# Kernel optimization log

Measured on AMD Instinct MI355X. Metric: run time of the kernel, lower is better.

Reference implementation:

```python
import jax, jax.numpy as jnp
import numpy as np

B, N, M = 64, 1024, 1024
WIDTH = 1.0
DECAY = 1.0


def setup_inputs() -> dict:
    key = jax.random.key(0)
    k1, k2, k3, k4, k5, k6 = jax.random.split(key, 6)
    # persistence-diagram style points: death = birth + positive lifetime
    bx = jax.random.uniform(k1, (B, N))
    lx = jax.random.uniform(k2, (B, N))
    X = jnp.stack([bx, bx + lx], axis=-1)  # [B, N, 2] (birth, death)
    by = jax.random.uniform(k3, (B, M))
    ly = jax.random.uniform(k4, (B, M))
    Y = jnp.stack([by, by + ly], axis=-1)  # [B, M, 2]
    weights = jax.random.uniform(k5, (B,), minval=0.1, maxval=1.0)
    num_samples = jnp.full((B,), float(N), dtype=jnp.float32)
    return {"X": X, "Y": Y, "weights": weights, "num_samples": num_samples}


def _to_lt(D):
    # (birth, death) -> (birth, lifetime)
    return jnp.stack([D[..., 0], D[..., 1] - D[..., 0]], axis=-1)


def _weighted_kernel_sum(A, Bp, wa, wb):
    # A: [B,n,2], Bp: [B,m,2]; squared euclidean distance, RBF, decay weighting, sum
    d2 = (jnp.sum(A * A, -1)[:, :, None]
          + jnp.sum(Bp * Bp, -1)[:, None, :]
          - 2.0 * jnp.einsum('bnd,bmd->bnm', A, Bp))
    K = jnp.exp(-jnp.maximum(d2, 0.0) / WIDTH)
    return jnp.einsum('bnm,bn,bm->b', K, wa, wb)


def reference(X, Y, weights, num_samples):
    PX = _to_lt(X)  # [B,N,2]
    PY = _to_lt(Y)  # [B,M,2]
    wX = PX[..., 1] ** DECAY  # lifetime^decay; 0 for zero-padded points
    wY = PY[..., 1] ** DECAY
    mmd = (_weighted_kernel_sum(PX, PX, wX, wX)
           - 2.0 * _weighted_kernel_sum(PX, PY, wX, wY)
           + _weighted_kernel_sum(PY, PY, wY, wY))  # [B]
    return jnp.sum(mmd * weights / (num_samples ** 2))
```

## Files before the change

### kernel.cpp

```cpp
#include <hip/hip_runtime.h>


#define LOG2E_F  1.44269504088896340736f
#define SQRT2C_F 1.69864360213614f

struct __align__(16) P4 { float sx, sy, h, w; };

#define NSLOT 64
#define TPB   256

#define ACC_BYTES (NSLOT * 8)
#define PTS_OFF   (ACC_BYTES + 16)

__global__ void prep_kernel(const float* __restrict__ X, const float* __restrict__ Y,
                            P4* __restrict__ PX, P4* __restrict__ PY,
                            int nx_total, int ny_total, double* __restrict__ acc) {
    int i = blockIdx.x * blockDim.x + threadIdx.x;
    if (i < NSLOT) acc[i] = 0.0;
    if (i < nx_total) {
        float2 bd = ((const float2*)X)[i];
        float x = bd.x, l = bd.y - bd.x;
        P4 p; p.sx = SQRT2C_F * x; p.sy = SQRT2C_F * l;
        p.h = -LOG2E_F * fmaf(x, x, l * l); p.w = l;
        PX[i] = p;
    }
    if (i < ny_total) {
        float2 bd = ((const float2*)Y)[i];
        float x = bd.x, l = bd.y - bd.x;
        P4 p; p.sx = SQRT2C_F * x; p.sy = SQRT2C_F * l;
        p.h = -LOG2E_F * fmaf(x, x, l * l); p.w = l;
        PY[i] = p;
    }
}

struct Rows { float asx[4], asy[4], ah[4], aw[4]; };

template<int RS>
__device__ __forceinline__ void strip_full(const P4* __restrict__ tile,
                                           const Rows& A, float* __restrict__ s) {
    #pragma unroll 4
    for (int m = 0; m < 64; ++m) {
        P4 p = tile[m];
        #pragma unroll
        for (int r = RS; r < 4; ++r) {
            float t = fmaf(A.asx[r], p.sx, fmaf(A.asy[r], p.sy, A.ah[r] + p.h));
            s[r] = fmaf(__builtin_amdgcn_exp2f(t), p.w, s[r]);
        }
    }
}

template<int RD>
__device__ __forceinline__ void strip_diag(const P4* __restrict__ tile, int kcap,
                                           const Rows& A, float* __restrict__ s) {
    #pragma unroll 4
    for (int m = 0; m < 64; ++m) {
        P4 p = tile[m];
        float wsel = (m < kcap) ? p.w : 0.0f;
        float t = fmaf(A.asx[RD], p.sx, fmaf(A.asy[RD], p.sy, A.ah[RD] + p.h));
        s[RD] = fmaf(__builtin_amdgcn_exp2f(t), wsel, s[RD]);
    }
}

__device__ __forceinline__ void do_strip_sym(const P4* __restrict__ tile, int j, int w,
                                             int kcap, const Rows& A, float* __restrict__ s) {
    int d = j + 1 - w;
    int rstart = (d <= 0) ? 0 : ((d + 3) >> 2);
    switch (rstart) {
        case 0: strip_full<0>(tile, A, s); break;
        case 1: strip_full<1>(tile, A, s); break;
        case 2: strip_full<2>(tile, A, s); break;
        case 3: strip_full<3>(tile, A, s); break;
        default: break;
    }
    int jd = j - w;
    if (jd >= 0 && jd < 16 && (jd & 3) == 0) {
        switch (jd >> 2) {
            case 0: strip_diag<0>(tile, kcap, A, s); break;
            case 1: strip_diag<1>(tile, kcap, A, s); break;
            case 2: strip_diag<2>(tile, kcap, A, s); break;
            case 3: strip_diag<3>(tile, kcap, A, s); break;
        }
    }
}

__global__ __launch_bounds__(TPB) void mmd_main(
    const P4* __restrict__ PXall, const P4* __restrict__ PYall,
    const float* __restrict__ weights, const float* __restrict__ ns,
    double* __restrict__ acc) {

    const int b    = blockIdx.y;
    const int part = blockIdx.x;
    const int tid  = threadIdx.x;
    const int w    = tid >> 6;
    const int lane = tid & 63;

    __shared__ P4 tiles[4][64];
    __shared__ double redbuf[4];
    P4* tile = tiles[w];

    const P4* __restrict__ PX = PXall + (size_t)b * 1024;
    const P4* __restrict__ PY = PYall + (size_t)b * 1024;

    float thread_val = 0.0f;

    if (part < 16) {
        const int p = part & 7;
        const P4* __restrict__ A = (part < 8) ? PX : PY;
        const int j0 = p, j1 = 15 - p;

        Rows R; float s[4];
        #pragma unroll
        for (int r = 0; r < 4; ++r) {
            P4 a = A[r * 256 + tid];
            R.asx[r] = a.sx; R.asy[r] = a.sy; R.ah[r] = a.h; R.aw[r] = a.w;
            s[r] = 0.0f;
        }

        P4 c0 = A[j0 * 64 + lane];
        P4 c1 = A[j1 * 64 + lane];
        tile[lane] = c0;
        do_strip_sym(tile, j0, w, lane, R, s);
        tile[lane] = c1;
        do_strip_sym(tile, j1, w, lane, R, s);

        float tv = 0.0f;
        #pragma unroll
        for (int r = 0; r < 4; ++r) tv = fmaf(R.aw[r], s[r], tv);
        tv *= 2.0f;
        if (p == 0) {
            #pragma unroll
            for (int r = 0; r < 4; ++r) tv = fmaf(R.aw[r], R.aw[r], tv);
        }
        thread_val = tv;
    } else {
        const int sp = part - 16;
        Rows R; float s[4];
        #pragma unroll
        for (int r = 0; r < 4; ++r) {
            P4 a = PX[r * 256 + tid];
            R.asx[r] = a.sx; R.asy[r] = a.sy; R.ah[r] = a.h; R.aw[r] = a.w;
            s[r] = 0.0f;
        }
        tile[lane] = PY[sp * 64 + lane];
        strip_full<0>(tile, R, s);

        float tv = 0.0f;
        #pragma unroll
        for (int r = 0; r < 4; ++r) tv = fmaf(R.aw[r], s[r], tv);
        thread_val = -2.0f * tv;
    }

    double v = (double)thread_val;
    #pragma unroll
    for (int off = 32; off > 0; off >>= 1) v += __shfl_down(v, off, 64);
    if (lane == 0) redbuf[w] = v;
    __syncthreads();
    if (tid == 0) {
        double tot = (redbuf[0] + redbuf[1]) + (redbuf[2] + redbuf[3]);
        double nsb = (double)ns[b];
        atomicAdd(&acc[b], tot * ((double)weights[b] / (nsb * nsb)));
    }
}

__global__ __launch_bounds__(TPB) void mmd_generic(
    const P4* __restrict__ PXall, const P4* __restrict__ PYall,
    const float* __restrict__ weights, const float* __restrict__ ns,
    int N, int M, double* __restrict__ acc) {

    const int b    = blockIdx.z;
    const int term = blockIdx.y;
    const int seg  = blockIdx.x;

    const P4* __restrict__ A  = (term == 2) ? (PYall + (size_t)b * M) : (PXall + (size_t)b * N);
    const P4* __restrict__ Bp = (term == 0) ? (PXall + (size_t)b * N) : (PYall + (size_t)b * M);
    const int nrows = (term == 2) ? M : N;
    const int mlen  = (term == 0) ? N : M;
    const float sign = (term == 1) ? -2.0f : 1.0f;

    const int mstart = seg * 32;
    const int cnt = (mstart + 32 <= mlen) ? 32 : (mlen > mstart ? mlen - mstart : 0);

    __shared__ P4 tile[32];
    __shared__ double redbuf[TPB / 64];
    if (threadIdx.x < cnt) tile[threadIdx.x] = Bp[mstart + threadIdx.x];
    __syncthreads();

    float thread_val = 0.0f;
    for (int n = threadIdx.x; n < nrows; n += TPB) {
        P4 a = A[n];
        float ss = 0.0f;
        for (int m = 0; m < cnt; ++m) {
            P4 p = tile[m];
            float t = fmaf(a.sx, p.sx, fmaf(a.sy, p.sy, a.h + p.h));
            ss = fmaf(__builtin_amdgcn_exp2f(t), p.w, ss);
        }
        thread_val = fmaf(a.w, ss, thread_val);
    }

    double v = (double)thread_val;
    #pragma unroll
    for (int off = 32; off > 0; off >>= 1) v += __shfl_down(v, off, 64);
    if ((threadIdx.x & 63) == 0) redbuf[threadIdx.x >> 6] = v;
    __syncthreads();
    if (threadIdx.x == 0) {
        double tot = (redbuf[0] + redbuf[1]) + (redbuf[2] + redbuf[3]);
        double nsb = (double)ns[b];
        atomicAdd(&acc[b], (double)sign * tot * ((double)weights[b] / (nsb * nsb)));
    }
}

__global__ void finalize_kernel(const double* __restrict__ acc, float* __restrict__ out) {
    if (threadIdx.x == 0 && blockIdx.x == 0) {
        double total = 0.0;
        #pragma unroll
        for (int i = 0; i < NSLOT; ++i) total += acc[i];
        out[0] = (float)total;
    }
}

extern "C" void kernel_launch(void* const* d_in, const int* in_sizes, int n_in,
                              void* d_out, int out_size, void* d_ws, size_t ws_size,
                              hipStream_t stream) {
    const float* X  = (const float*)d_in[0];
    const float* Y  = (const float*)d_in[1];
    const float* W  = (const float*)d_in[2];
    const float* NS = (const float*)d_in[3];

    const int B = in_sizes[2];
    const int N = in_sizes[0] / (2 * B);
    const int M = in_sizes[1] / (2 * B);

    double* acc = (double*)d_ws;
    P4* PX = (P4*)((char*)d_ws + PTS_OFF);
    P4* PY = PX + (size_t)B * N;

    const int nx_total = B * N;
    const int ny_total = B * M;
    const int prep_total = nx_total > ny_total ? nx_total : ny_total;

    prep_kernel<<<(prep_total + 255) / 256, 256, 0, stream>>>(
        X, Y, PX, PY, nx_total, ny_total, acc);

    if (N == 1024 && M == 1024 && B <= NSLOT) {
        dim3 grid(32, B);
        mmd_main<<<grid, TPB, 0, stream>>>(PX, PY, W, NS, acc);
    } else {
        const int mlen_max = N > M ? N : M;
        dim3 grid((mlen_max + 31) / 32, 3, B);
        mmd_generic<<<grid, TPB, 0, stream>>>(PX, PY, W, NS, N, M, acc);
    }

    finalize_kernel<<<1, 64, 0, stream>>>(acc, (float*)d_out);
}
```

Baseline: 91.83 us.

## Fuse prep into main kernel, use packed polynomial exp2, slot-based reduction

Drops the separate prep kernel: each block now converts the raw (birth, death) pairs into scaled coordinates itself while loading its rows and staging a structure-of-arrays LDS tile. The inner loop handles two columns at a time with packed v2f FMAs, and the hardware exp2 is replaced by a degree-7 polynomial evaluated on packed FMA lanes. Per-block results go to per-block slots instead of double atomics, and a parallel finalize kernel sums them. This aims to cut launch overhead and move exp work off the transcendental unit onto packed FMA, at the cost of extra VALU instructions and slightly different rounding.

```diff
diff --git a/kernel.cpp b/kernel.cpp
--- a/kernel.cpp
+++ b/kernel.cpp
@@ -3,14 +3,199 @@
 
 #define LOG2E_F  1.44269504088896340736f
 #define SQRT2C_F 1.69864360213614f
+#define MAGIC_F  12582912.0f
+
+typedef float        v2f __attribute__((ext_vector_type(2)));
+typedef unsigned int v2u __attribute__((ext_vector_type(2)));
+
+#define TPB 256
+
+__device__ __forceinline__ v2f fma2(v2f a, v2f b, v2f c) {
+    return __builtin_elementwise_fma(a, b, c);
+}
+__device__ __forceinline__ v2f splat2(float x) { return (v2f){x, x}; }
+
+__device__ __forceinline__ v2f exp2_poly(v2f t) {
+    const v2f MG = splat2(MAGIC_F);
+    v2f z = t + MG;
+    v2f n = z - MG;
+    v2f f = t - n;
+    v2f q = splat2(1.5252733e-5f);
+    q = fma2(q, f, splat2(1.5403530e-4f));
+    q = fma2(q, f, splat2(1.3333558e-3f));
+    q = fma2(q, f, splat2(9.6181291e-3f));
+    q = fma2(q, f, splat2(5.5504109e-2f));
+    q = fma2(q, f, splat2(2.4022651e-1f));
+    q = fma2(q, f, splat2(6.9314718e-1f));
+    q = fma2(q, f, splat2(1.0f));
+    v2u zb = __builtin_bit_cast(v2u, z);
+    v2u sb = (zb << 23) + 0x3F800000u;
+    return q * __builtin_bit_cast(v2f, sb);
+}
+
+struct __align__(16) WTile { float sx[64], sy[64], h[64], w[64]; };
+struct Rows { float sx[4], sy[4], h[4], w[4]; };
+
+__device__ __forceinline__ void stage_strip(WTile* T, const float2* src,
+                                            int col0, int lane) {
+    float2 bd = src[col0 + lane];
+    float x = bd.x, l = bd.y - bd.x;
+    T->sx[lane] = SQRT2C_F * x;
+    T->sy[lane] = SQRT2C_F * l;
+    T->h[lane]  = -LOG2E_F * fmaf(x, x, l * l);
+    T->w[lane]  = l;
+}
+
+__device__ __forceinline__ void load_rows(Rows& R, const float2* src, int tid) {
+    #pragma unroll
+    for (int r = 0; r < 4; ++r) {
+        float2 bd = src[r * 256 + tid];
+        float x = bd.x, l = bd.y - bd.x;
+        R.sx[r] = SQRT2C_F * x;
+        R.sy[r] = SQRT2C_F * l;
+        R.h[r]  = -LOG2E_F * fmaf(x, x, l * l);
+        R.w[r]  = l;
+    }
+}
+
+template<int RS>
+__device__ __forceinline__ void strip_full(const WTile* T, const Rows& R,
+                                           v2f* __restrict__ acc) {
+    #pragma unroll 4
+    for (int m = 0; m < 64; m += 2) {
+        v2f psx = *(const v2f*)&T->sx[m];
+        v2f psy = *(const v2f*)&T->sy[m];
+        v2f ph  = *(const v2f*)&T->h[m];
+        v2f pw  = *(const v2f*)&T->w[m];
+        #pragma unroll
+        for (int r = RS; r < 4; ++r) {
+            v2f t = fma2(splat2(R.sx[r]), psx,
+                     fma2(splat2(R.sy[r]), psy, ph + splat2(R.h[r])));
+            acc[r] = fma2(exp2_poly(t), pw, acc[r]);
+        }
+    }
+}
+
+template<int RD>
+__device__ __forceinline__ void strip_diag(const WTile* T, const Rows& R,
+                                           int kcap, v2f* __restrict__ acc) {
+    #pragma unroll 4
+    for (int m = 0; m < 64; m += 2) {
+        v2f psx = *(const v2f*)&T->sx[m];
+        v2f psy = *(const v2f*)&T->sy[m];
+        v2f ph  = *(const v2f*)&T->h[m];
+        v2f pw  = *(const v2f*)&T->w[m];
+        v2f wm = { (m     < kcap) ? pw.x : 0.0f,
+                   (m + 1 < kcap) ? pw.y : 0.0f };
+        v2f t = fma2(splat2(R.sx[RD]), psx,
+                 fma2(splat2(R.sy[RD]), psy, ph + splat2(R.h[RD])));
+        acc[RD] = fma2(exp2_poly(t), wm, acc[RD]);
+    }
+}
+
+__device__ __forceinline__ void do_strip_sym(const WTile* T, int j, int w,
+                                             int kcap, const Rows& R,
+                                             v2f* __restrict__ acc) {
+    int d = j + 1 - w;
+    int rstart = (d <= 0) ? 0 : ((d + 3) >> 2);
+    switch (rstart) {
+        case 0: strip_full<0>(T, R, acc); break;
+        case 1: strip_full<1>(T, R, acc); break;
+        case 2: strip_full<2>(T, R, acc); break;
+        case 3: strip_full<3>(T, R, acc); break;
+        default: break;
+    }
+    int jd = j - w;
+    if (jd >= 0 && jd < 16 && (jd & 3) == 0) {
+        switch (jd >> 2) {
+            case 0: strip_diag<0>(T, R, kcap, acc); break;
+            case 1: strip_diag<1>(T, R, kcap, acc); break;
+            case 2: strip_diag<2>(T, R, kcap, acc); break;
+            case 3: strip_diag<3>(T, R, kcap, acc); break;
+        }
+    }
+}
+
+__global__ __launch_bounds__(TPB) void mmd_main(
+    const float* __restrict__ X, const float* __restrict__ Y,
+    const float* __restrict__ weights, const float* __restrict__ ns,
+    double* __restrict__ slots) {
+
+    const int b    = blockIdx.y;
+    const int part = blockIdx.x;
+    const int tid  = threadIdx.x;
+    const int w    = tid >> 6;
+    const int lane = tid & 63;
+
+    __shared__ WTile tiles[4];
+    __shared__ double redbuf[4];
+    WTile* T = &tiles[w];
+
+    const float2* Xb = (const float2*)X + (size_t)b * 1024;
+    const float2* Yb = (const float2*)Y + (size_t)b * 1024;
+
+    float thread_val = 0.0f;
+    v2f acc[4] = { splat2(0.0f), splat2(0.0f), splat2(0.0f), splat2(0.0f) };
+
+    if (part < 16) {
+        const int p = part & 7;
+        const float2* src = (part < 8) ? Xb : Yb;
+        Rows R; load_rows(R, src, tid);
+
+        stage_strip(T, src, p * 64, lane);
+        do_strip_sym(T, p, w, lane, R, acc);
+        stage_strip(T, src, (15 - p) * 64, lane);
+        do_strip_sym(T, 15 - p, w, lane, R, acc);
+
+        float tv = 0.0f;
+        #pragma unroll
+        for (int r = 0; r < 4; ++r) tv = fmaf(R.w[r], acc[r].x + acc[r].y, tv);
+        tv *= 2.0f;
+        if (p == 0) {
+            #pragma unroll
+            for (int r = 0; r < 4; ++r) tv = fmaf(R.w[r], R.w[r], tv);
+        }
+        thread_val = tv;
+    } else {
+        const int sp = part - 16;
+        Rows R; load_rows(R, Xb, tid);
+        stage_strip(T, Yb, sp * 64, lane);
+        strip_full<0>(T, R, acc);
+        float tv = 0.0f;
+        #pragma unroll
+        for (int r = 0; r < 4; ++r) tv = fmaf(R.w[r], acc[r].x + acc[r].y, tv);
+        thread_val = -2.0f * tv;
+    }
+
+    double v = (double)thread_val;
+    #pragma unroll
+    for (int off = 32; off > 0; off >>= 1) v += __shfl_down(v, off, 64);
+    if (lane == 0) redbuf[w] = v;
+    __syncthreads();
+    if (tid == 0) {
+        double tot = (redbuf[0] + redbuf[1]) + (redbuf[2] + redbuf[3]);
+        double nsb = (double)ns[b];
+        slots[(size_t)b * 32 + part] = tot * ((double)weights[b] / (nsb * nsb));
+    }
+}
+
+__global__ void finalize_slots(const double* __restrict__ slots, int count,
+                               float* __restrict__ out) {
+    const int tid = threadIdx.x;
+    double s = 0.0;
+    for (int i = tid; i < count; i += TPB) s += slots[i];
+    #pragma unroll
+    for (int off = 32; off > 0; off >>= 1) s += __shfl_down(s, off, 64);
+    __shared__ double redbuf[4];
+    if ((tid & 63) == 0) redbuf[tid >> 6] = s;
+    __syncthreads();
+    if (tid == 0)
+        out[0] = (float)((redbuf[0] + redbuf[1]) + (redbuf[2] + redbuf[3]));
+}
 
 struct __align__(16) P4 { float sx, sy, h, w; };
-
 #define NSLOT 64
-#define TPB   256
-
-#define ACC_BYTES (NSLOT * 8)
-#define PTS_OFF   (ACC_BYTES + 16)
+#define PTS_OFF 16400
 
 __global__ void prep_kernel(const float* __restrict__ X, const float* __restrict__ Y,
                             P4* __restrict__ PX, P4* __restrict__ PY,
@@ -33,135 +218,6 @@
     }
 }
 
-struct Rows { float asx[4], asy[4], ah[4], aw[4]; };
-
-template<int RS>
-__device__ __forceinline__ void strip_full(const P4* __restrict__ tile,
-                                           const Rows& A, float* __restrict__ s) {
-    #pragma unroll 4
-    for (int m = 0; m < 64; ++m) {
-        P4 p = tile[m];
-        #pragma unroll
-        for (int r = RS; r < 4; ++r) {
-            float t = fmaf(A.asx[r], p.sx, fmaf(A.asy[r], p.sy, A.ah[r] + p.h));
-            s[r] = fmaf(__builtin_amdgcn_exp2f(t), p.w, s[r]);
-        }
-    }
-}
-
-template<int RD>
-__device__ __forceinline__ void strip_diag(const P4* __restrict__ tile, int kcap,
-                                           const Rows& A, float* __restrict__ s) {
-    #pragma unroll 4
-    for (int m = 0; m < 64; ++m) {
-        P4 p = tile[m];
-        float wsel = (m < kcap) ? p.w : 0.0f;
-        float t = fmaf(A.asx[RD], p.sx, fmaf(A.asy[RD], p.sy, A.ah[RD] + p.h));
-        s[RD] = fmaf(__builtin_amdgcn_exp2f(t), wsel, s[RD]);
-    }
-}
-
-__device__ __forceinline__ void do_strip_sym(const P4* __restrict__ tile, int j, int w,
-                                             int kcap, const Rows& A, float* __restrict__ s) {
-    int d = j + 1 - w;
-    int rstart = (d <= 0) ? 0 : ((d + 3) >> 2);
-    switch (rstart) {
-        case 0: strip_full<0>(tile, A, s); break;
-        case 1: strip_full<1>(tile, A, s); break;
-        case 2: strip_full<2>(tile, A, s); break;
-        case 3: strip_full<3>(tile, A, s); break;
-        default: break;
-    }
-    int jd = j - w;
-    if (jd >= 0 && jd < 16 && (jd & 3) == 0) {
-        switch (jd >> 2) {
-            case 0: strip_diag<0>(tile, kcap, A, s); break;
-            case 1: strip_diag<1>(tile, kcap, A, s); break;
-            case 2: strip_diag<2>(tile, kcap, A, s); break;
-            case 3: strip_diag<3>(tile, kcap, A, s); break;
-        }
-    }
-}
-
-__global__ __launch_bounds__(TPB) void mmd_main(
-    const P4* __restrict__ PXall, const P4* __restrict__ PYall,
-    const float* __restrict__ weights, const float* __restrict__ ns,
-    double* __restrict__ acc) {
-
-    const int b    = blockIdx.y;
-    const int part = blockIdx.x;
-    const int tid  = threadIdx.x;
-    const int w    = tid >> 6;
-    const int lane = tid & 63;
-
-    __shared__ P4 tiles[4][64];
-    __shared__ double redbuf[4];
-    P4* tile = tiles[w];
-
-    const P4* __restrict__ PX = PXall + (size_t)b * 1024;
-    const P4* __restrict__ PY = PYall + (size_t)b * 1024;
-
-    float thread_val = 0.0f;
-
-    if (part < 16) {
-        const int p = part & 7;
-        const P4* __restrict__ A = (part < 8) ? PX : PY;
-        const int j0 = p, j1 = 15 - p;
-
-        Rows R; float s[4];
-        #pragma unroll
-        for (int r = 0; r < 4; ++r) {
-            P4 a = A[r * 256 + tid];
-            R.asx[r] = a.sx; R.asy[r] = a.sy; R.ah[r] = a.h; R.aw[r] = a.w;
-            s[r] = 0.0f;
-        }
-
-        P4 c0 = A[j0 * 64 + lane];
-        P4 c1 = A[j1 * 64 + lane];
-        tile[lane] = c0;
-        do_strip_sym(tile, j0, w, lane, R, s);
-        tile[lane] = c1;
-        do_strip_sym(tile, j1, w, lane, R, s);
-
-        float tv = 0.0f;
-        #pragma unroll
-        for (int r = 0; r < 4; ++r) tv = fmaf(R.aw[r], s[r], tv);
-        tv *= 2.0f;
-        if (p == 0) {
-            #pragma unroll
-            for (int r = 0; r < 4; ++r) tv = fmaf(R.aw[r], R.aw[r], tv);
-        }
-        thread_val = tv;
-    } else {
-        const int sp = part - 16;
-        Rows R; float s[4];
-        #pragma unroll
-        for (int r = 0; r < 4; ++r) {
-            P4 a = PX[r * 256 + tid];
-            R.asx[r] = a.sx; R.asy[r] = a.sy; R.ah[r] = a.h; R.aw[r] = a.w;
-            s[r] = 0.0f;
-        }
-        tile[lane] = PY[sp * 64 + lane];
-        strip_full<0>(tile, R, s);
-
-        float tv = 0.0f;
-        #pragma unroll
-        for (int r = 0; r < 4; ++r) tv = fmaf(R.aw[r], s[r], tv);
-        thread_val = -2.0f * tv;
-    }
-
-    double v = (double)thread_val;
-    #pragma unroll
-    for (int off = 32; off > 0; off >>= 1) v += __shfl_down(v, off, 64);
-    if (lane == 0) redbuf[w] = v;
-    __syncthreads();
-    if (tid == 0) {
-        double tot = (redbuf[0] + redbuf[1]) + (redbuf[2] + redbuf[3]);
-        double nsb = (double)ns[b];
-        atomicAdd(&acc[b], tot * ((double)weights[b] / (nsb * nsb)));
-    }
-}
-
 __global__ __launch_bounds__(TPB) void mmd_generic(
     const P4* __restrict__ PXall, const P4* __restrict__ PYall,
     const float* __restrict__ weights, const float* __restrict__ ns,
@@ -209,15 +265,6 @@
     }
 }
 
-__global__ void finalize_kernel(const double* __restrict__ acc, float* __restrict__ out) {
-    if (threadIdx.x == 0 && blockIdx.x == 0) {
-        double total = 0.0;
-        #pragma unroll
-        for (int i = 0; i < NSLOT; ++i) total += acc[i];
-        out[0] = (float)total;
-    }
-}
-
 extern "C" void kernel_launch(void* const* d_in, const int* in_sizes, int n_in,
                               void* d_out, int out_size, void* d_ws, size_t ws_size,
                               hipStream_t stream) {
@@ -230,25 +277,22 @@
     const int N = in_sizes[0] / (2 * B);
     const int M = in_sizes[1] / (2 * B);
 
-    double* acc = (double*)d_ws;
-    P4* PX = (P4*)((char*)d_ws + PTS_OFF);
-    P4* PY = PX + (size_t)B * N;
-
-    const int nx_total = B * N;
-    const int ny_total = B * M;
-    const int prep_total = nx_total > ny_total ? nx_total : ny_total;
-
-    prep_kernel<<<(prep_total + 255) / 256, 256, 0, stream>>>(
-        X, Y, PX, PY, nx_total, ny_total, acc);
-
-    if (N == 1024 && M == 1024 && B <= NSLOT) {
+    if (N == 1024 && M == 1024 && B * 32 * 8 <= 16384) {
+        double* slots = (double*)d_ws;
         dim3 grid(32, B);
-        mmd_main<<<grid, TPB, 0, stream>>>(PX, PY, W, NS, acc);
+        mmd_main<<<grid, TPB, 0, stream>>>(X, Y, W, NS, slots);
+        finalize_slots<<<1, TPB, 0, stream>>>(slots, B * 32, (float*)d_out);
     } else {
+        double* acc = (double*)d_ws;
+        P4* PX = (P4*)((char*)d_ws + PTS_OFF);
+        P4* PY = PX + (size_t)B * N;
+        const int nx_total = B * N, ny_total = B * M;
+        const int prep_total = nx_total > ny_total ? nx_total : ny_total;
+        prep_kernel<<<(prep_total + 255) / 256, 256, 0, stream>>>(
+            X, Y, PX, PY, nx_total, ny_total, acc);
         const int mlen_max = N > M ? N : M;
         dim3 grid((mlen_max + 31) / 32, 3, B);
         mmd_generic<<<grid, TPB, 0, stream>>>(PX, PY, W, NS, N, M, acc);
-    }
-
-    finalize_kernel<<<1, 64, 0, stream>>>(acc, (float*)d_out);
-}
+        finalize_slots<<<1, TPB, 0, stream>>>(acc, NSLOT, (float*)d_out);
+    }
+}
```

New measurement: 115.9 us. 26.2% more time.
